# Performance work log

Measured on AMD Instinct MI355X. Metric: run time of the kernel, lower is better.

The kernel has to match this reference:

```python
import jax, jax.numpy as jnp
import numpy as np

B, S, CIN, WIDTH, COUT = 8, 256, 3, 64, 1
MODES, BW = 32, 3


def _dct_matrix(n):
    # orthonormal DCT-II matrix; inverse = transpose (DCT-III)
    k = np.arange(n)[:, None].astype(np.float64)
    x = np.arange(n)[None, :].astype(np.float64)
    m = np.sqrt(2.0 / n) * np.cos(np.pi * (x + 0.5) * k / n)
    m[0] *= 1.0 / np.sqrt(2.0)
    return jnp.asarray(m, dtype=jnp.float32)

DCT = _dct_matrix(S)  # [S, S]


def T_fwd(u):  # u: [B, C, H, W] -> spectral coefficients
    u = jnp.einsum('kh,bchw->bckw', DCT, u)
    return jnp.einsum('lw,bckw->bckl', DCT, u)


def T_inv(c):  # inverse transform (orthonormal => transpose)
    c = jnp.einsum('kh,bckw->bchw', DCT, c)
    return jnp.einsum('lw,bclw->bclh', DCT, c).transpose(0, 1, 3, 2)


def T_inv2(c):
    # straightforward version: apply M^T along both spatial dims
    c = jnp.einsum('kh,bckl->bchl', DCT, c)
    return jnp.einsum('lw,bchl->bchw', DCT, c)


def gelu(x):
    return jax.nn.gelu(x, approximate=False)


def pseudo_spectra(u, w, cout):
    # u: [B, Cin, S, S]; w: [Cin*BW*BW, cout, MODES*MODES]
    b = T_fwd(u)
    p = MODES + BW - 1
    bp = b[:, :, :p, :p]  # pad_slices (triL=0)
    # im2col matching torch.nn.Unfold channel-major ordering (c, ki, kj)
    patches = jnp.stack([bp[:, :, i:i + MODES, j:j + MODES]
                         for i in range(BW) for j in range(BW)], axis=2)
    bs, cin = u.shape[0], u.shape[1]
    xp = patches.reshape(bs, cin * BW * BW, MODES * MODES)
    om = jnp.einsum('bix,iox->box', xp, w).reshape(bs, cout, MODES, MODES)
    out = jnp.zeros((bs, cout, S, S), u.dtype).at[:, :, :MODES, :MODES].set(om)
    return T_inv2(out)


def conv1x1(x, w, b):
    return jnp.einsum('oi,bihw->bohw', w, x) + b[None, :, None, None]


def setup_inputs() -> dict:
    key = jax.random.key(0)
    ks = jax.random.split(key, 20)
    mm = MODES * MODES
    inp = {'x': jax.random.normal(ks[0], (B, S, S, CIN), dtype=jnp.float32)}
    # PseudoSpectra weights: scale * U[0,1), scale = 1/(in*out)
    inp['wl'] = jax.random.uniform(ks[1], (CIN * BW * BW, WIDTH - CIN, mm), dtype=jnp.float32) / (CIN * (WIDTH - CIN))
    for i in range(4):
        inp[f'wc{i}'] = jax.random.uniform(ks[2 + i], (WIDTH * BW * BW, WIDTH, mm), dtype=jnp.float32) / (WIDTH * WIDTH)
    for i in range(4):
        inp[f'pw{i}'] = jax.random.normal(ks[6 + i], (WIDTH, WIDTH), dtype=jnp.float32) * 0.05
        inp[f'pb{i}'] = jnp.zeros((WIDTH,), dtype=jnp.float32)
    inp['fc1_w'] = jax.random.normal(ks[10], (WIDTH, 128), dtype=jnp.float32) * 0.05
    inp['fc1_b'] = jnp.zeros((128,), dtype=jnp.float32)
    inp['fc2_w'] = jax.random.normal(ks[11], (128, COUT), dtype=jnp.float32) * 0.05
    inp['fc2_b'] = jnp.zeros((COUT,), dtype=jnp.float32)
    return inp


def reference(x, wl, wc0, wc1, wc2, wc3,
              pw0, pb0, pw1, pb1, pw2, pb2, pw3, pb3,
              fc1_w, fc1_b, fc2_w, fc2_b):
    h = x.transpose(0, 3, 1, 2)  # [B, CIN, S, S]
    h = jnp.concatenate([h, gelu(pseudo_spectra(h, wl, WIDTH - CIN))], axis=1)
    h = h + gelu(conv1x1(h, pw0, pb0) + pseudo_spectra(h, wc0, WIDTH))
    h = h + gelu(conv1x1(h, pw1, pb1) + pseudo_spectra(h, wc1, WIDTH))
    h = h + gelu(conv1x1(h, pw2, pb2) + pseudo_spectra(h, wc2, WIDTH))
    h = h + gelu(conv1x1(h, pw3, pb3) + pseudo_spectra(h, wc3, WIDTH))
    h = h.transpose(0, 2, 3, 1)  # [B, S, S, WIDTH]
    h = gelu(h @ fc1_w + fc1_b)
    h = h @ fc2_w + fc2_b  # [B, S, S, COUT]
    y = h.transpose(0, 3, 1, 2)
    y = T_fwd(T_inv2(y))  # T(T.inv(.)) along spatial dims, as in source
    return y.transpose(0, 2, 3, 1)
```

## Files before the change

kernel.cpp:

```cpp
#include <hip/hip_runtime.h>
#include <math.h>

#define BB 8
#define S 256
#define CIN 3
#define W64 64
#define MODES 32
#define PP 34
#define KPAD 36
#define KPB 40

typedef __attribute__((ext_vector_type(8))) short bfrag;
typedef __attribute__((ext_vector_type(16))) float f32x16;

__device__ __forceinline__ float gelu_f(float x){
    float z = fabsf(x) * 0.70710678118654752f;
    float t = 1.0f / (1.0f + 0.3275911f * z);
    float p = ((((1.061405429f * t - 1.453152027f) * t) + 1.421413741f) * t
               - 0.284496736f) * t + 0.254829592f;
    float e = __expf(-z * z);
    float erf = 1.0f - p * t * e;
    erf = copysignf(erf, x);
    return 0.5f * x * (1.0f + erf);
}

__device__ __forceinline__ void split_bf(float x, short &hi, short &lo){
    unsigned u = __float_as_uint(x);
    unsigned r = u + 0x7FFFu + ((u >> 16) & 1u);
    hi = (short)(r >> 16);
    float hf = __uint_as_float(r & 0xFFFF0000u);
    float l = x - hf;
    unsigned v = __float_as_uint(l);
    unsigned s2 = v + 0x7FFFu + ((v >> 16) & 1u);
    lo = (short)(s2 >> 16);
}

__device__ __forceinline__ void split8(float4 a, float4 b, bfrag &hv, bfrag &lv){
    short hi, lo;
    split_bf(a.x, hi, lo); hv[0] = hi; lv[0] = lo;
    split_bf(a.y, hi, lo); hv[1] = hi; lv[1] = lo;
    split_bf(a.z, hi, lo); hv[2] = hi; lv[2] = lo;
    split_bf(a.w, hi, lo); hv[3] = hi; lv[3] = lo;
    split_bf(b.x, hi, lo); hv[4] = hi; lv[4] = lo;
    split_bf(b.y, hi, lo); hv[5] = hi; lv[5] = lo;
    split_bf(b.z, hi, lo); hv[6] = hi; lv[6] = lo;
    split_bf(b.w, hi, lo); hv[7] = hi; lv[7] = lo;
}

__device__ __forceinline__ float bf2f(short s){
    return __uint_as_float(((unsigned)(unsigned short)s) << 16);
}

__global__ void k_init_dt(float* __restrict__ dt, short* __restrict__ dth,
                          short* __restrict__ dtl){
    int tid = blockIdx.x * 256 + threadIdx.x;
    if (tid >= S * KPB) return;
    int h = tid / KPB, k = tid % KPB;
    double v = 0.0;
    if (k < PP) {
        v = sqrt(2.0 / (double)S) * cos(3.14159265358979323846 * (h + 0.5) * k / (double)S);
        if (k == 0) v *= 0.70710678118654752440;
    }
    float f = (float)v;
    if (k < KPAD) dt[h * KPAD + k] = f;
    short hi, lo; split_bf(f, hi, lo);
    dth[tid] = hi; dtl[tid] = lo;
}

__global__ void k_prep_pw(const float* __restrict__ pw, short* __restrict__ pwh,
                          short* __restrict__ pwl){
    int e = blockIdx.x * 256 + threadIdx.x;
    if (e >= 4096) return;
    short hi, lo; split_bf(pw[e], hi, lo);
    pwh[e] = hi; pwl[e] = lo;
}

__global__ void k_prep_fc1(const float* __restrict__ fc1w, short* __restrict__ f1h,
                           short* __restrict__ f1l){
    int e = blockIdx.x * 256 + threadIdx.x;
    if (e >= 8192) return;
    int i = e >> 7, j = e & 127;
    int n = j >> 5, ks = i >> 4;
    int l = (j & 31) + (((i & 15) >= 8) ? 32 : 0);
    int jr = i & 7;
    int idx = ((n * 4 + ks) * 64 + l) * 8 + jr;
    short hi, lo; split_bf(fc1w[e], hi, lo);
    f1h[idx] = hi; f1l[idx] = lo;
}

__global__ void k_copy_x(const float* __restrict__ x, float* __restrict__ h){
    int e = blockIdx.x * 256 + threadIdx.x;
    if (e >= BB * S * S * CIN) return;
    int px = e / CIN, c = e % CIN;
    h[(size_t)px * W64 + c] = x[e];
}

template<int C>
__global__ void k_fwd1(const float* __restrict__ src, float* __restrict__ tmp1,
                       const float* __restrict__ dt){
    int b = blockIdx.y;
    int idx = blockIdx.x * 256 + threadIdx.x;
    if (idx >= S * C) return;
    float acc[PP];
    #pragma unroll
    for (int k = 0; k < PP; k++) acc[k] = 0.f;
    const float* sp = src + (size_t)b * S * S * C + idx;
    for (int hh = 0; hh < S; hh++){
        float v = sp[(size_t)hh * S * C];
        const float* dr = dt + hh * KPAD;
        #pragma unroll
        for (int k = 0; k < PP; k++) acc[k] = fmaf(dr[k], v, acc[k]);
    }
    float* op = tmp1 + (size_t)b * PP * S * C + idx;
    #pragma unroll
    for (int k = 0; k < PP; k++) op[(size_t)k * S * C] = acc[k];
}

__global__ void k_fwd1_64s(const float* __restrict__ src, float* __restrict__ tmp1,
                           const float* __restrict__ dt){
    const int C = 64;
    const size_t TM1 = (size_t)BB * PP * S * C;
    int b = blockIdx.z, hf = blockIdx.y;
    int idx = blockIdx.x * 256 + threadIdx.x;
    float acc[PP];
    #pragma unroll
    for (int k = 0; k < PP; k++) acc[k] = 0.f;
    const float* sp = src + (size_t)b * S * S * C + (size_t)hf * 128 * S * C + idx;
    for (int hh = 0; hh < 128; hh++){
        float v = sp[(size_t)hh * S * C];
        const float* dr = dt + (hf * 128 + hh) * KPAD;
        #pragma unroll
        for (int k = 0; k < PP; k++) acc[k] = fmaf(dr[k], v, acc[k]);
    }
    float* op = tmp1 + (size_t)hf * TM1 + (size_t)b * PP * S * C + idx;
    #pragma unroll
    for (int k = 0; k < PP; k++) op[(size_t)k * S * C] = acc[k];
}

__global__ void k_fwd2_3(const float* __restrict__ tmp1, float* __restrict__ bp,
                         const float* __restrict__ dt){
    const int C = 3;
    int b = blockIdx.y;
    int idx = blockIdx.x * 256 + threadIdx.x;
    if (idx >= PP * C) return;
    int k = idx / C, c = idx % C;
    float acc[PP];
    #pragma unroll
    for (int l = 0; l < PP; l++) acc[l] = 0.f;
    const float* sp = tmp1 + ((size_t)b * PP + k) * S * C + c;
    for (int w = 0; w < S; w++){
        float v = sp[(size_t)w * C];
        const float* dr = dt + w * KPAD;
        #pragma unroll
        for (int l = 0; l < PP; l++) acc[l] = fmaf(dr[l], v, acc[l]);
    }
    float* op = bp + ((size_t)b * PP + k) * PP * C + c;
    #pragma unroll
    for (int l = 0; l < PP; l++) op[(size_t)l * C] = acc[l];
}

__global__ __launch_bounds__(256, 4) void k_fwd2_64(
        const float* __restrict__ tmp1, float* __restrict__ bp,
        const float* __restrict__ dt){
    const int C = 64;
    const size_t TM1 = (size_t)BB * PP * S * C;
    __shared__ float red[4 * PP * 66];
    int k = blockIdx.x, b = blockIdx.y;
    int t = threadIdx.x;
    int c = t & 63;
    int ws = __builtin_amdgcn_readfirstlane(t >> 6);
    float acc[PP];
    #pragma unroll
    for (int l = 0; l < PP; l++) acc[l] = 0.f;
    const float* sp = tmp1 + ((size_t)b * PP + k) * S * C + c;
    for (int w = ws * 64; w < ws * 64 + 64; w++){
        float v = sp[(size_t)w * C] + sp[TM1 + (size_t)w * C];
        const float* dr = dt + w * KPAD;
        #pragma unroll
        for (int l = 0; l < PP; l++) acc[l] = fmaf(dr[l], v, acc[l]);
    }
    #pragma unroll
    for (int l = 0; l < PP; l++) red[(ws * PP + l) * 66 + c] = acc[l];
    __syncthreads();
    float* op = bp + ((size_t)b * PP + k) * PP * C;
    for (int e = t; e < PP * C; e += 256){
        int l = e >> 6, cc = e & 63;
        op[e] = red[(0 * PP + l) * 66 + cc] + red[(1 * PP + l) * 66 + cc]
              + red[(2 * PP + l) * 66 + cc] + red[(3 * PP + l) * 66 + cc];
    }
}

template<int C, int CC>
__global__ void k_xp_gather(const float* __restrict__ bp, float* __restrict__ xp){
    __shared__ float lds[8 * 3 * PP * (CC + 1)];
    int k  = blockIdx.x;
    int c0 = blockIdx.y * CC;
    int t  = threadIdx.x;
    const int TOT = 8 * 3 * PP * CC;
    for (int e = t; e < TOT; e += 256){
        int b   = e / (3 * PP * CC);
        int r   = e % (3 * PP * CC);
        int row = r / (PP * CC);
        int r2  = r % (PP * CC);
        int l   = r2 / CC;
        int c   = r2 % CC;
        lds[((b * 3 + row) * PP + l) * (CC + 1) + c] =
            bp[(((size_t)b * PP + (k + row)) * PP + l) * C + c0 + c];
    }
    __syncthreads();
    int l = t >> 3;
    int b = t & 7;
    for (int c = 0; c < CC; c++){
        #pragma unroll
        for (int ij = 0; ij < 9; ij++){
            int i_ = ij / 3, j_ = ij % 3;
            int i  = (c0 + c) * 9 + ij;
            float v = lds[((b * 3 + i_) * PP + (l + j_)) * (CC + 1) + c];
            xp[((size_t)i * 1024 + k * 32 + l) * 8 + b] = v;
        }
    }
}

template<int ITOT, int O>
__global__ void k_om(const float* __restrict__ xp, const float* __restrict__ w,
                     float* __restrict__ part){
    int bx  = blockIdx.x;
    int klt = bx & 31;
    int ot  = (bx >> 5) & 7;
    int ns  = bx >> 8;
    const int ILEN = ITOT / 3;
    int t  = threadIdx.x;
    int kl = klt * 32 + (t & 31);
    int o  = ot * 8 + (t >> 5);
    if (o >= O) return;
    float a0=0,a1=0,a2=0,a3=0,a4=0,a5=0,a6=0,a7=0;
    const float* xpp = xp + ((size_t)(ns * ILEN) * 1024 + kl) * 8;
    const float* wp  = w + ((size_t)(ns * ILEN) * O + o) * 1024 + kl;
    #pragma unroll 4
    for (int i = 0; i < ILEN; i++){
        float4 xa = *(const float4*)(xpp + (size_t)i * 8192);
        float4 xb = *(const float4*)(xpp + (size_t)i * 8192 + 4);
        float wv  = wp[(size_t)i * O * 1024];
        a0 = fmaf(xa.x, wv, a0); a1 = fmaf(xa.y, wv, a1);
        a2 = fmaf(xa.z, wv, a2); a3 = fmaf(xa.w, wv, a3);
        a4 = fmaf(xb.x, wv, a4); a5 = fmaf(xb.y, wv, a5);
        a6 = fmaf(xb.z, wv, a6); a7 = fmaf(xb.w, wv, a7);
    }
    float* pp = part + (size_t)ns * 8 * 64 * 1024;
    pp[((size_t)0 * 64 + o) * 1024 + kl] = a0;
    pp[((size_t)1 * 64 + o) * 1024 + kl] = a1;
    pp[((size_t)2 * 64 + o) * 1024 + kl] = a2;
    pp[((size_t)3 * 64 + o) * 1024 + kl] = a3;
    pp[((size_t)4 * 64 + o) * 1024 + kl] = a4;
    pp[((size_t)5 * 64 + o) * 1024 + kl] = a5;
    pp[((size_t)6 * 64 + o) * 1024 + kl] = a6;
    pp[((size_t)7 * 64 + o) * 1024 + kl] = a7;
}

template<int O>
__global__ void k_inv1(const float* __restrict__ part, float* __restrict__ t2,
                       const float* __restrict__ dt){
    __shared__ float oms[32 * 65];
    const int N = 8 * 64 * 1024;
    int wc = blockIdx.x, k = blockIdx.y, b = blockIdx.z;
    int t = threadIdx.x;
    for (int e = t; e < 2048; e += 256){
        int o_ = e >> 5, l = e & 31;
        int idx = ((b * 64 + o_) << 10) + k * 32 + l;
        oms[l * 65 + o_] = part[idx] + part[N + idx] + part[2 * N + idx];
    }
    __syncthreads();
    int o  = t & 63;
    int wg = __builtin_amdgcn_readfirstlane(t >> 6);
    int wbase = wc * 32 + wg * 8;
    float acc[8];
    #pragma unroll
    for (int wj = 0; wj < 8; wj++) acc[wj] = 0.f;
    for (int l = 0; l < 32; l++){
        float ov = oms[l * 65 + o];
        #pragma unroll
        for (int wj = 0; wj < 8; wj++)
            acc[wj] = fmaf(dt[(wbase + wj) * KPAD + l], ov, acc[wj]);
    }
    if (o < O){
        #pragma unroll
        for (int wj = 0; wj < 8; wj++)
            t2[(((size_t)b * 32 + k) * S + wbase + wj) * 64 + o] = acc[wj];
    }
}

template<bool CONV>
__global__ __launch_bounds__(256, 3) void k_fused(
        const float* __restrict__ t2, float* __restrict__ h,
        const short* __restrict__ pwh, const short* __restrict__ pwl,
        const float* __restrict__ pb,
        const short* __restrict__ dth, const short* __restrict__ dtl){
    __shared__ short t2fh[8 * 64 * 8];
    __shared__ short t2fl[8 * 64 * 8];
    __shared__ short hsfh[CONV ? 2 * 8 * 64 * 8 : 1];
    __shared__ short hsfl[CONV ? 2 * 8 * 64 * 8 : 1];
    int wt = blockIdx.x, b = blockIdx.y;
    int t = threadIdx.x;

    #pragma unroll
    for (int e2 = 0; e2 < 2; e2++){
        int e = t + e2 * 256;
        int le = e & 63, ks = (e >> 6) & 1, ne = e >> 7;
        int oe = (ne & 1) * 32 + (le & 31);
        int we = wt * 2 + (ne >> 1);
        int k0 = ks * 16 + (le >> 5) * 8;
        bfrag hv, lv;
        #pragma unroll
        for (int j = 0; j < 8; j++){
            short hi, lo;
            split_bf(t2[((size_t)(b * 32 + k0 + j) * S + we) * 64 + oe], hi, lo);
            hv[j] = hi; lv[j] = lo;
        }
        int idx = ((ne * 2 + ks) * 64 + le) * 8;
        *(bfrag*)(t2fh + idx) = hv;
        *(bfrag*)(t2fl + idx) = lv;
    }

    int l = t & 63;
    int n = t >> 6;
    int oh = n & 1, wl = n >> 1;
    int o = oh * 32 + (l & 31);

    int g_res = wl * 4 + (o >> 4);
    int jres  = o & 7;
    int rowadd = ((o & 15) >= 8) ? 32 : 0;

    int ihalf = t & 7;
    int pxA = t >> 3;
    int pxB = pxA + 32;
    const float* hb = h + ((size_t)b * S * S + (size_t)wt * 2) * 64;
    size_t offA = ((size_t)(pxA >> 1) * S + (pxA & 1)) * 64 + ihalf * 8;
    size_t offB = ((size_t)(pxB >> 1) * S + (pxB & 1)) * 64 + ihalf * 8;
    float4 a0, a1, b0, b1;
    if (CONV){
        a0 = *(const float4*)(hb + offA);
        a1 = *(const float4*)(hb + offA + 4);
        b0 = *(const float4*)(hb + offB);
        b1 = *(const float4*)(hb + offB + 4);
    }

    int cur = 0;
    for (int ht = 0; ht < 8; ht++){
        if (CONV){
            int ks = ihalf >> 1;
            int lh = (ihalf & 1) * 32;
            int g  = (pxA & 1) * 4 + ks;
            bfrag hv, lv;
            split8(a0, a1, hv, lv);
            int rowA = (pxA >> 1) + lh;
            *(bfrag*)(hsfh + cur * 4096 + (g * 64 + (rowA ^ g)) * 8) = hv;
            *(bfrag*)(hsfl + cur * 4096 + (g * 64 + (rowA ^ g)) * 8) = lv;
            split8(b0, b1, hv, lv);
            int rowB = (pxB >> 1) + lh;
            *(bfrag*)(hsfh + cur * 4096 + (g * 64 + (rowB ^ g)) * 8) = hv;
            *(bfrag*)(hsfl + cur * 4096 + (g * 64 + (rowB ^ g)) * 8) = lv;
            __syncthreads();
        } else {
            if (ht == 0) __syncthreads();
        }
        if (CONV && ht < 7){
            const float* hb2 = hb + (size_t)(ht + 1) * 32 * S * 64;
            a0 = *(const float4*)(hb2 + offA);
            a1 = *(const float4*)(hb2 + offA + 4);
            b0 = *(const float4*)(hb2 + offB);
            b1 = *(const float4*)(hb2 + offB + 4);
        }

        f32x16 acc = {0,0,0,0,0,0,0,0,0,0,0,0,0,0,0,0};

        int hh0 = ht * 32;
        #pragma unroll
        for (int ks = 0; ks < 2; ks++){
            int aoff = (hh0 + (l & 31)) * KPB + ks * 16 + (l >> 5) * 8;
            bfrag ah = *(const bfrag*)(dth + aoff);
            bfrag al = *(const bfrag*)(dtl + aoff);
            int boff = ((n * 2 + ks) * 64 + l) * 8;
            bfrag bh = *(const bfrag*)(t2fh + boff);
            bfrag bl = *(const bfrag*)(t2fl + boff);
            acc = __builtin_amdgcn_mfma_f32_32x32x16_bf16(ah, bh, acc, 0, 0, 0);
            acc = __builtin_amdgcn_mfma_f32_32x32x16_bf16(ah, bl, acc, 0, 0, 0);
            acc = __builtin_amdgcn_mfma_f32_32x32x16_bf16(al, bh, acc, 0, 0, 0);
        }

        if (CONV){
            #pragma unroll
            for (int ks = 0; ks < 4; ks++){
                int g = wl * 4 + ks;
                int aoff = cur * 4096 + (g * 64 + (l ^ g)) * 8;
                bfrag ah = *(const bfrag*)(hsfh + aoff);
                bfrag al = *(const bfrag*)(hsfl + aoff);
                int boff = o * 64 + ks * 16 + (l >> 5) * 8;
                bfrag bh = *(const bfrag*)(pwh + boff);
                bfrag bl = *(const bfrag*)(pwl + boff);
                acc = __builtin_amdgcn_mfma_f32_32x32x16_bf16(ah, bh, acc, 0, 0, 0);
                acc = __builtin_amdgcn_mfma_f32_32x32x16_bf16(ah, bl, acc, 0, 0, 0);
                acc = __builtin_amdgcn_mfma_f32_32x32x16_bf16(al, bh, acc, 0, 0, 0);
            }
            float pbv = pb[o];
            #pragma unroll
            for (int r = 0; r < 16; r++){
                int row = (r & 3) + 8 * (r >> 2) + 4 * (l >> 5);
                int ei = cur * 4096 + (g_res * 64 + ((row + rowadd) ^ g_res)) * 8 + jres;
                float res = bf2f(hsfh[ei]) + bf2f(hsfl[ei]);
                size_t pix = ((size_t)b * S + ht * 32 + row) * S + wt * 2 + wl;
                h[pix * 64 + o] = res + gelu_f(acc[r] + pbv);
            }
            cur ^= 1;
        } else {
            if (o < 61){
                #pragma unroll
                for (int r = 0; r < 16; r++){
                    int row = (r & 3) + 8 * (r >> 2) + 4 * (l >> 5);
                    size_t pix = ((size_t)b * S + ht * 32 + row) * S + wt * 2 + wl;
                    h[pix * 64 + 3 + o] = gelu_f(acc[r]);
                }
            }
        }
    }
}

__global__ __launch_bounds__(256, 4) void k_mlp(
        const float* __restrict__ h, const short* __restrict__ f1h,
        const short* __restrict__ f1l, const float* __restrict__ fc1b,
        const float* __restrict__ fc2w, const float* __restrict__ fc2b,
        float* __restrict__ out){
    __shared__ short ah_[2 * 4 * 64 * 8];
    __shared__ short al_[2 * 4 * 64 * 8];
    __shared__ float red[2 * 64 * 33];
    size_t base = (size_t)blockIdx.x * 64;
    int t = threadIdx.x;
    const float* hrow = h + base * 64;
    #pragma unroll
    for (int e2 = 0; e2 < 2; e2++){
        int e = t + e2 * 256;
        int px = e >> 3, ih = e & 7;
        float4 v0 = *(const float4*)(hrow + px * 64 + ih * 8);
        float4 v1 = *(const float4*)(hrow + px * 64 + ih * 8 + 4);
        bfrag hv, lv;
        split8(v0, v1, hv, lv);
        int g = (px >> 5) * 4 + (ih >> 1);
        int row = (px & 31) + (ih & 1) * 32;
        *(bfrag*)(ah_ + (g * 64 + (row ^ g)) * 8) = hv;
        *(bfrag*)(al_ + (g * 64 + (row ^ g)) * 8) = lv;
    }
    __syncthreads();
    int l = t & 63;
    int w = t >> 6;
    int m = w >> 1;
    int n0 = (w & 1) * 2;
    f32x16 acc0 = {0,0,0,0,0,0,0,0,0,0,0,0,0,0,0,0};
    f32x16 acc1 = {0,0,0,0,0,0,0,0,0,0,0,0,0,0,0,0};
    #pragma unroll
    for (int ks = 0; ks < 4; ks++){
        int g = m * 4 + ks;
        int aoff = (g * 64 + (l ^ g)) * 8;
        bfrag ah = *(const bfrag*)(ah_ + aoff);
        bfrag al = *(const bfrag*)(al_ + aoff);
        int b0off = ((n0 * 4 + ks) * 64 + l) * 8;
        int b1off = (((n0 + 1) * 4 + ks) * 64 + l) * 8;
        bfrag b0h = *(const bfrag*)(f1h + b0off);
        bfrag b0l = *(const bfrag*)(f1l + b0off);
        bfrag b1h = *(const bfrag*)(f1h + b1off);
        bfrag b1l = *(const bfrag*)(f1l + b1off);
        acc0 = __builtin_amdgcn_mfma_f32_32x32x16_bf16(ah, b0h, acc0, 0, 0, 0);
        acc0 = __builtin_amdgcn_mfma_f32_32x32x16_bf16(ah, b0l, acc0, 0, 0, 0);
        acc0 = __builtin_amdgcn_mfma_f32_32x32x16_bf16(al, b0h, acc0, 0, 0, 0);
        acc1 = __builtin_amdgcn_mfma_f32_32x32x16_bf16(ah, b1h, acc1, 0, 0, 0);
        acc1 = __builtin_amdgcn_mfma_f32_32x32x16_bf16(ah, b1l, acc1, 0, 0, 0);
        acc1 = __builtin_amdgcn_mfma_f32_32x32x16_bf16(al, b1h, acc1, 0, 0, 0);
    }
    int j0 = n0 * 32 + (l & 31), j1 = j0 + 32;
    float b10 = fc1b[j0], b11 = fc1b[j1];
    float f20 = fc2w[j0], f21 = fc2w[j1];
    float* rb = red + (w & 1) * 64 * 33;
    #pragma unroll
    for (int r = 0; r < 16; r++){
        int row = (r & 3) + 8 * (r >> 2) + 4 * (l >> 5);
        rb[(m * 32 + row) * 33 + (l & 31)] =
            gelu_f(acc0[r] + b10) * f20 + gelu_f(acc1[r] + b11) * f21;
    }
    __syncthreads();
    if (t < 64){
        float s = fc2b[0];
        #pragma unroll
        for (int c = 0; c < 32; c++)
            s += red[t * 33 + c] + red[(64 + t) * 33 + c];
        out[base + t] = s;
    }
}

extern "C" void kernel_launch(void* const* d_in, const int* in_sizes, int n_in,
                              void* d_out, int out_size, void* d_ws, size_t ws_size,
                              hipStream_t stream) {
    const float* x    = (const float*)d_in[0];
    const float* wl   = (const float*)d_in[1];
    const float* wc[4] = {(const float*)d_in[2], (const float*)d_in[3],
                          (const float*)d_in[4], (const float*)d_in[5]};
    const float* pw[4] = {(const float*)d_in[6], (const float*)d_in[8],
                          (const float*)d_in[10], (const float*)d_in[12]};
    const float* pb[4] = {(const float*)d_in[7], (const float*)d_in[9],
                          (const float*)d_in[11], (const float*)d_in[13]};
    const float* fc1w = (const float*)d_in[14];
    const float* fc1b = (const float*)d_in[15];
    const float* fc2w = (const float*)d_in[16];
    const float* fc2b = (const float*)d_in[17];
    float* out = (float*)d_out;

    char* ws = (char*)d_ws;
    size_t off = 0;
    float* dt   = (float*)(ws + off); off += (size_t)S * KPAD * 4;
    short* dth  = (short*)(ws + off); off += (size_t)S * KPB * 2;
    short* dtl  = (short*)(ws + off); off += (size_t)S * KPB * 2;
    short* pwh  = (short*)(ws + off); off += (size_t)4 * 4096 * 2;
    short* pwl  = (short*)(ws + off); off += (size_t)4 * 4096 * 2;
    short* f1h  = (short*)(ws + off); off += (size_t)8192 * 2;
    short* f1l  = (short*)(ws + off); off += (size_t)8192 * 2;
    float* h    = (float*)(ws + off); off += (size_t)BB * S * S * W64 * 4;
    float* tmp1 = (float*)(ws + off); off += (size_t)2 * BB * PP * S * W64 * 4;
    float* bp   = (float*)(ws + off); off += (size_t)BB * PP * PP * W64 * 4;
    float* xp   = (float*)(ws + off); off += (size_t)576 * 1024 * 8 * 4;
    float* part = (float*)(ws + off); off += (size_t)3 * 8 * 64 * 1024 * 4;
    float* t2   = (float*)(ws + off); off += (size_t)BB * 32 * S * W64 * 4;

    k_init_dt<<<(S * KPB + 255) / 256, 256, 0, stream>>>(dt, dth, dtl);
    for (int i = 0; i < 4; i++)
        k_prep_pw<<<16, 256, 0, stream>>>(pw[i], pwh + i * 4096, pwl + i * 4096);
    k_prep_fc1<<<32, 256, 0, stream>>>(fc1w, f1h, f1l);
    k_copy_x<<<(BB * S * S * CIN + 255) / 256, 256, 0, stream>>>(x, h);

    k_fwd1<3><<<dim3(3, BB), 256, 0, stream>>>(x, tmp1, dt);
    k_fwd2_3<<<dim3(1, BB), 256, 0, stream>>>(tmp1, bp, dt);
    k_xp_gather<3, 3><<<dim3(32, 1), 256, 0, stream>>>(bp, xp);
    k_om<27, 61><<<768, 256, 0, stream>>>(xp, wl, part);
    k_inv1<61><<<dim3(8, 32, BB), 256, 0, stream>>>(part, t2, dt);
    k_fused<false><<<dim3(128, BB), 256, 0, stream>>>(
        t2, h, nullptr, nullptr, nullptr, dth, dtl);

    for (int blk = 0; blk < 4; blk++){
        k_fwd1_64s<<<dim3(64, 2, BB), 256, 0, stream>>>(h, tmp1, dt);
        k_fwd2_64<<<dim3(PP, BB), 256, 0, stream>>>(tmp1, bp, dt);
        k_xp_gather<64, 16><<<dim3(32, 4), 256, 0, stream>>>(bp, xp);
        k_om<576, 64><<<768, 256, 0, stream>>>(xp, wc[blk], part);
        k_inv1<64><<<dim3(8, 32, BB), 256, 0, stream>>>(part, t2, dt);
        k_fused<true><<<dim3(128, BB), 256, 0, stream>>>(
            t2, h, pwh + blk * 4096, pwl + blk * 4096, pb[blk], dth, dtl);
    }

    k_mlp<<<dim3(BB * S * S / 64), 256, 0, stream>>>(h, f1h, f1l, fc1b, fc2w, fc2b, out);
}
```

Measured before the change: 1.172 ms.

## Split fused inverse-DCT/conv kernel across row tiles with swizzled 1D grid

The fused kernel no longer loops over 8 row tiles inside each block. It launches 8192 blocks with a swizzled index mapping, so each block handles one (batch, column-tile, row-tile). This raises parallelism from 1024 to 8192 blocks and halves the shared-memory buffers. In exchange, every block reloads and re-splits its t2 tile, 8x redundant, and loses the software-pipelined prefetch of the next h tile. It also raises wave priority around the MFMA section.

```diff
diff --git a/kernel.cpp b/kernel.cpp
--- a/kernel.cpp
+++ b/kernel.cpp
@@ -297,9 +297,13 @@
         const short* __restrict__ dth, const short* __restrict__ dtl){
     __shared__ short t2fh[8 * 64 * 8];
     __shared__ short t2fl[8 * 64 * 8];
-    __shared__ short hsfh[CONV ? 2 * 8 * 64 * 8 : 1];
-    __shared__ short hsfl[CONV ? 2 * 8 * 64 * 8 : 1];
-    int wt = blockIdx.x, b = blockIdx.y;
+    __shared__ short hsfh[CONV ? 8 * 64 * 8 : 1];
+    __shared__ short hsfl[CONV ? 8 * 64 * 8 : 1];
+    int bid = blockIdx.x;
+    int swz = (bid & 7) * 1024 + (bid >> 3);
+    int b  = swz >> 10;
+    int wt = (swz >> 3) & 127;
+    int ht = swz & 7;
     int t = threadIdx.x;
 
     #pragma unroll
@@ -321,104 +325,90 @@
         *(bfrag*)(t2fl + idx) = lv;
     }
 
+    if (CONV){
+        int ihalf = t & 7;
+        int pxA = t >> 3;
+        int pxB = pxA + 32;
+        const float* hb = h + (((size_t)b * S + ht * 32) * S + (size_t)wt * 2) * 64;
+        size_t offA = ((size_t)(pxA >> 1) * S + (pxA & 1)) * 64 + ihalf * 8;
+        size_t offB = ((size_t)(pxB >> 1) * S + (pxB & 1)) * 64 + ihalf * 8;
+        float4 a0 = *(const float4*)(hb + offA);
+        float4 a1 = *(const float4*)(hb + offA + 4);
+        float4 b0 = *(const float4*)(hb + offB);
+        float4 b1 = *(const float4*)(hb + offB + 4);
+        int ks = ihalf >> 1;
+        int lh = (ihalf & 1) * 32;
+        int g  = (pxA & 1) * 4 + ks;
+        bfrag hv, lv;
+        split8(a0, a1, hv, lv);
+        int rowA = (pxA >> 1) + lh;
+        *(bfrag*)(hsfh + (g * 64 + (rowA ^ g)) * 8) = hv;
+        *(bfrag*)(hsfl + (g * 64 + (rowA ^ g)) * 8) = lv;
+        split8(b0, b1, hv, lv);
+        int rowB = (pxB >> 1) + lh;
+        *(bfrag*)(hsfh + (g * 64 + (rowB ^ g)) * 8) = hv;
+        *(bfrag*)(hsfl + (g * 64 + (rowB ^ g)) * 8) = lv;
+    }
+    __syncthreads();
+
     int l = t & 63;
     int n = t >> 6;
     int oh = n & 1, wl = n >> 1;
     int o = oh * 32 + (l & 31);
 
-    int g_res = wl * 4 + (o >> 4);
-    int jres  = o & 7;
-    int rowadd = ((o & 15) >= 8) ? 32 : 0;
-
-    int ihalf = t & 7;
-    int pxA = t >> 3;
-    int pxB = pxA + 32;
-    const float* hb = h + ((size_t)b * S * S + (size_t)wt * 2) * 64;
-    size_t offA = ((size_t)(pxA >> 1) * S + (pxA & 1)) * 64 + ihalf * 8;
-    size_t offB = ((size_t)(pxB >> 1) * S + (pxB & 1)) * 64 + ihalf * 8;
-    float4 a0, a1, b0, b1;
+    f32x16 acc = {0,0,0,0,0,0,0,0,0,0,0,0,0,0,0,0};
+
+    __builtin_amdgcn_s_setprio(1);
+    int hh0 = ht * 32;
+    #pragma unroll
+    for (int ks = 0; ks < 2; ks++){
+        int aoff = (hh0 + (l & 31)) * KPB + ks * 16 + (l >> 5) * 8;
+        bfrag ah = *(const bfrag*)(dth + aoff);
+        bfrag al = *(const bfrag*)(dtl + aoff);
+        int boff = ((n * 2 + ks) * 64 + l) * 8;
+        bfrag bh = *(const bfrag*)(t2fh + boff);
+        bfrag bl = *(const bfrag*)(t2fl + boff);
+        acc = __builtin_amdgcn_mfma_f32_32x32x16_bf16(ah, bh, acc, 0, 0, 0);
+        acc = __builtin_amdgcn_mfma_f32_32x32x16_bf16(ah, bl, acc, 0, 0, 0);
+        acc = __builtin_amdgcn_mfma_f32_32x32x16_bf16(al, bh, acc, 0, 0, 0);
+    }
     if (CONV){
-        a0 = *(const float4*)(hb + offA);
-        a1 = *(const float4*)(hb + offA + 4);
-        b0 = *(const float4*)(hb + offB);
-        b1 = *(const float4*)(hb + offB + 4);
-    }
-
-    int cur = 0;
-    for (int ht = 0; ht < 8; ht++){
-        if (CONV){
-            int ks = ihalf >> 1;
-            int lh = (ihalf & 1) * 32;
-            int g  = (pxA & 1) * 4 + ks;
-            bfrag hv, lv;
-            split8(a0, a1, hv, lv);
-            int rowA = (pxA >> 1) + lh;
-            *(bfrag*)(hsfh + cur * 4096 + (g * 64 + (rowA ^ g)) * 8) = hv;
-            *(bfrag*)(hsfl + cur * 4096 + (g * 64 + (rowA ^ g)) * 8) = lv;
-            split8(b0, b1, hv, lv);
-            int rowB = (pxB >> 1) + lh;
-            *(bfrag*)(hsfh + cur * 4096 + (g * 64 + (rowB ^ g)) * 8) = hv;
-            *(bfrag*)(hsfl + cur * 4096 + (g * 64 + (rowB ^ g)) * 8) = lv;
-            __syncthreads();
-        } else {
-            if (ht == 0) __syncthreads();
-        }
-        if (CONV && ht < 7){
-            const float* hb2 = hb + (size_t)(ht + 1) * 32 * S * 64;
-            a0 = *(const float4*)(hb2 + offA);
-            a1 = *(const float4*)(hb2 + offA + 4);
-            b0 = *(const float4*)(hb2 + offB);
-            b1 = *(const float4*)(hb2 + offB + 4);
-        }
-
-        f32x16 acc = {0,0,0,0,0,0,0,0,0,0,0,0,0,0,0,0};
-
-        int hh0 = ht * 32;
-        #pragma unroll
-        for (int ks = 0; ks < 2; ks++){
-            int aoff = (hh0 + (l & 31)) * KPB + ks * 16 + (l >> 5) * 8;
-            bfrag ah = *(const bfrag*)(dth + aoff);
-            bfrag al = *(const bfrag*)(dtl + aoff);
-            int boff = ((n * 2 + ks) * 64 + l) * 8;
-            bfrag bh = *(const bfrag*)(t2fh + boff);
-            bfrag bl = *(const bfrag*)(t2fl + boff);
+        #pragma unroll
+        for (int ks = 0; ks < 4; ks++){
+            int g = wl * 4 + ks;
+            int aoff = (g * 64 + (l ^ g)) * 8;
+            bfrag ah = *(const bfrag*)(hsfh + aoff);
+            bfrag al = *(const bfrag*)(hsfl + aoff);
+            int boff = o * 64 + ks * 16 + (l >> 5) * 8;
+            bfrag bh = *(const bfrag*)(pwh + boff);
+            bfrag bl = *(const bfrag*)(pwl + boff);
             acc = __builtin_amdgcn_mfma_f32_32x32x16_bf16(ah, bh, acc, 0, 0, 0);
             acc = __builtin_amdgcn_mfma_f32_32x32x16_bf16(ah, bl, acc, 0, 0, 0);
             acc = __builtin_amdgcn_mfma_f32_32x32x16_bf16(al, bh, acc, 0, 0, 0);
         }
-
-        if (CONV){
-            #pragma unroll
-            for (int ks = 0; ks < 4; ks++){
-                int g = wl * 4 + ks;
-                int aoff = cur * 4096 + (g * 64 + (l ^ g)) * 8;
-                bfrag ah = *(const bfrag*)(hsfh + aoff);
-                bfrag al = *(const bfrag*)(hsfl + aoff);
-                int boff = o * 64 + ks * 16 + (l >> 5) * 8;
-                bfrag bh = *(const bfrag*)(pwh + boff);
-                bfrag bl = *(const bfrag*)(pwl + boff);
-                acc = __builtin_amdgcn_mfma_f32_32x32x16_bf16(ah, bh, acc, 0, 0, 0);
-                acc = __builtin_amdgcn_mfma_f32_32x32x16_bf16(ah, bl, acc, 0, 0, 0);
-                acc = __builtin_amdgcn_mfma_f32_32x32x16_bf16(al, bh, acc, 0, 0, 0);
-            }
-            float pbv = pb[o];
+    }
+    __builtin_amdgcn_s_setprio(0);
+
+    if (CONV){
+        int g_res = wl * 4 + (o >> 4);
+        int jres  = o & 7;
+        int rowadd = ((o & 15) >= 8) ? 32 : 0;
+        float pbv = pb[o];
+        float* hout = h + (((size_t)b * S + ht * 32) * S + wt * 2 + wl) * 64 + o;
+        #pragma unroll
+        for (int r = 0; r < 16; r++){
+            int row = (r & 3) + 8 * (r >> 2) + 4 * (l >> 5);
+            int ei = (g_res * 64 + ((row + rowadd) ^ g_res)) * 8 + jres;
+            float res = bf2f(hsfh[ei]) + bf2f(hsfl[ei]);
+            hout[row * (S * 64)] = res + gelu_f(acc[r] + pbv);
+        }
+    } else {
+        if (o < 61){
+            float* hout = h + (((size_t)b * S + ht * 32) * S + wt * 2 + wl) * 64 + 3 + o;
             #pragma unroll
             for (int r = 0; r < 16; r++){
                 int row = (r & 3) + 8 * (r >> 2) + 4 * (l >> 5);
-                int ei = cur * 4096 + (g_res * 64 + ((row + rowadd) ^ g_res)) * 8 + jres;
-                float res = bf2f(hsfh[ei]) + bf2f(hsfl[ei]);
-                size_t pix = ((size_t)b * S + ht * 32 + row) * S + wt * 2 + wl;
-                h[pix * 64 + o] = res + gelu_f(acc[r] + pbv);
-            }
-            cur ^= 1;
-        } else {
-            if (o < 61){
-                #pragma unroll
-                for (int r = 0; r < 16; r++){
-                    int row = (r & 3) + 8 * (r >> 2) + 4 * (l >> 5);
-                    size_t pix = ((size_t)b * S + ht * 32 + row) * S + wt * 2 + wl;
-                    h[pix * 64 + 3 + o] = gelu_f(acc[r]);
-                }
+                hout[row * (S * 64)] = gelu_f(acc[r]);
             }
         }
     }
@@ -538,7 +528,7 @@
     k_xp_gather<3, 3><<<dim3(32, 1), 256, 0, stream>>>(bp, xp);
     k_om<27, 61><<<768, 256, 0, stream>>>(xp, wl, part);
     k_inv1<61><<<dim3(8, 32, BB), 256, 0, stream>>>(part, t2, dt);
-    k_fused<false><<<dim3(128, BB), 256, 0, stream>>>(
+    k_fused<false><<<dim3(8192), 256, 0, stream>>>(
         t2, h, nullptr, nullptr, nullptr, dth, dtl);
 
     for (int blk = 0; blk < 4; blk++){
@@ -547,7 +537,7 @@
         k_xp_gather<64, 16><<<dim3(32, 4), 256, 0, stream>>>(bp, xp);
         k_om<576, 64><<<768, 256, 0, stream>>>(xp, wc[blk], part);
         k_inv1<64><<<dim3(8, 32, BB), 256, 0, stream>>>(part, t2, dt);
-        k_fused<true><<<dim3(128, BB), 256, 0, stream>>>(
+        k_fused<true><<<dim3(8192), 256, 0, stream>>>(
             t2, h, pwh + blk * 4096, pwl + blk * 4096, pb[blk], dth, dtl);
     }
 
```

New measurement: 1.246 ms. 6.3% more time.
